# Performance work log

Measured on AMD Instinct MI355X. Metric: run time of the kernel, lower is better.

Reference implementation:

```python
import jax, jax.numpy as jnp
import numpy as np

DENSITY = 0.1  # fraction of nonzero weights kept by the mask


def setup_inputs() -> dict:
    key = jax.random.key(0)
    k_data, k_w, k_m, k_b = jax.random.split(key, 4)
    M, N, K = 8192, 4096, 4096  # tokens, out_features, in_features
    data = jax.random.normal(k_data, (M, K), dtype=jnp.float32)
    weight = jax.random.normal(k_w, (N, K), dtype=jnp.float32)
    mask = (jax.random.uniform(k_m, (N, K)) < DENSITY).astype(jnp.float32)
    bias = jax.random.normal(k_b, (N,), dtype=jnp.float32)
    return {"data": data, "weight": weight, "mask": mask, "bias": bias}


def reference(data, weight, mask, bias):
    # Equivalent to cuSPARSE CSR SpMM with W_sparse = mask * weight, plus bias:
    # out = data @ (mask * weight)^T + bias  (same math as ref_forward / F.linear)
    w = mask * weight  # [N, K]
    out = jnp.einsum('mk,nk->mn', data, w) + bias  # [M, N]
    return out
```

## Files before the change

### kernel.cpp

```cpp
#include <hip/hip_runtime.h>
#include <hip/hip_bf16.h>


#define Mdim 8192
#define Ndim 4096
#define Kdim 4096

typedef __bf16 bf16x8 __attribute__((ext_vector_type(8)));
typedef float f32x4 __attribute__((ext_vector_type(4)));

__device__ inline unsigned short f2bf(float f) {
    union { float f; unsigned u; } v;
    v.f = f;
    unsigned r = v.u + 0x7fffu + ((v.u >> 16) & 1u);
    return (unsigned short)(r >> 16);
}

__device__ inline unsigned pack2(float a, float b) {
    return (unsigned)f2bf(a) | ((unsigned)f2bf(b) << 16);
}

#define GLOAD_LDS16(gp, lp)                                                     \
    __builtin_amdgcn_global_load_lds((const __attribute__((address_space(1))) void*)(gp), \
                                     (__attribute__((address_space(3))) void*)(lp), 16, 0, 0)

__global__ __launch_bounds__(256) void k_cvt_all(const float4* __restrict__ data,
                                                 const float4* __restrict__ weight,
                                                 const float4* __restrict__ mask,
                                                 uint4* __restrict__ Abf,
                                                 uint4* __restrict__ Bbf) {
    const int NA = Mdim * (Kdim / 8);
    const int NB = Ndim * (Kdim / 8);
    const int stride = gridDim.x * blockDim.x;
    for (int i = blockIdx.x * blockDim.x + threadIdx.x; i < NA + NB; i += stride) {
        if (i < NA) {
            const size_t j2 = 2 * (size_t)i;
            float4 v0 = data[j2], v1 = data[j2 + 1];
            uint4 o;
            o.x = pack2(v0.x, v0.y); o.y = pack2(v0.z, v0.w);
            o.z = pack2(v1.x, v1.y); o.w = pack2(v1.z, v1.w);
            Abf[i] = o;
        } else {
            const size_t j = (size_t)(i - NA);
            const size_t j2 = 2 * j;
            float4 w0 = weight[j2], w1 = weight[j2 + 1];
            float4 m0 = mask[j2],   m1 = mask[j2 + 1];
            uint4 o;
            o.x = pack2(w0.x * m0.x, w0.y * m0.y);
            o.y = pack2(w0.z * m0.z, w0.w * m0.w);
            o.z = pack2(w1.x * m1.x, w1.y * m1.y);
            o.w = pack2(w1.z * m1.z, w1.w * m1.w);
            Bbf[j] = o;
        }
    }
}

__global__ __launch_bounds__(256) void k_gemm(const unsigned short* __restrict__ A,
                                              const unsigned short* __restrict__ B,
                                              const float* __restrict__ bias,
                                              float* __restrict__ out) {
    __shared__ unsigned short As[128 * 32];
    __shared__ unsigned short Bs[128 * 32];

    const int tid  = threadIdx.x;
    const int lane = tid & 63;
    const int wave = tid >> 6;
    const int wm   = (wave >> 1) * 64;
    const int wn   = (wave & 1) * 64;
    const int bm   = blockIdx.y * 128;
    const int bn   = blockIdx.x * 128;

    const int ar = lane >> 2;
    const int ac = (lane & 3) * 8;
    const unsigned short* Ag0 = A + (size_t)(bm + wave * 32 + ar) * Kdim + ac;
    const unsigned short* Ag1 = Ag0 + (size_t)16 * Kdim;
    const unsigned short* Bg0 = B + (size_t)(bn + wave * 32 + ar) * Kdim + ac;
    const unsigned short* Bg1 = Bg0 + (size_t)16 * Kdim;
    unsigned short* Al0 = As + wave * 1024 + lane * 8;
    unsigned short* Al1 = Al0 + 512;
    unsigned short* Bl0 = Bs + wave * 1024 + lane * 8;
    unsigned short* Bl1 = Bl0 + 512;

    f32x4 zero = {0.f, 0.f, 0.f, 0.f};
    f32x4 acc[4][4];
#pragma unroll
    for (int i = 0; i < 4; ++i)
#pragma unroll
        for (int j = 0; j < 4; ++j) acc[i][j] = zero;

    const int fr = lane & 15;
    const int fk = (lane >> 4) * 8;

    for (int k0 = 0; k0 < Kdim; k0 += 32) {
        GLOAD_LDS16(Ag0 + k0, Al0);
        GLOAD_LDS16(Ag1 + k0, Al1);
        GLOAD_LDS16(Bg0 + k0, Bl0);
        GLOAD_LDS16(Bg1 + k0, Bl1);
        __syncthreads();

        bf16x8 af[4], bfr[4];
#pragma unroll
        for (int i = 0; i < 4; ++i)
            af[i] = *(const bf16x8*)&As[(wm + i * 16 + fr) * 32 + fk];
#pragma unroll
        for (int j = 0; j < 4; ++j)
            bfr[j] = *(const bf16x8*)&Bs[(wn + j * 16 + fr) * 32 + fk];

#pragma unroll
        for (int i = 0; i < 4; ++i)
#pragma unroll
            for (int j = 0; j < 4; ++j)
                acc[i][j] = __builtin_amdgcn_mfma_f32_16x16x32_bf16(af[i], bfr[j], acc[i][j], 0, 0, 0);

        __syncthreads();
    }

    const int col_base = bn + wn + (lane & 15);
    const int row_base = bm + wm + (lane >> 4) * 4;
#pragma unroll
    for (int j = 0; j < 4; ++j) {
        const int col = col_base + j * 16;
        const float bv = bias[col];
#pragma unroll
        for (int i = 0; i < 4; ++i) {
            const int row = row_base + i * 16;
            float* op = out + (size_t)row * Ndim + col;
#pragma unroll
            for (int r = 0; r < 4; ++r) op[(size_t)r * Ndim] = acc[i][j][r] + bv;
        }
    }
}

__global__ void k_naive(const float* __restrict__ A, const float* __restrict__ W,
                        const float* __restrict__ Msk, const float* __restrict__ bias,
                        float* __restrict__ out) {
    int n = blockIdx.x * blockDim.x + threadIdx.x;
    int m = blockIdx.y;
    if (n >= Ndim) return;
    const float* a = A + (size_t)m * Kdim;
    const float* w = W + (size_t)n * Kdim;
    const float* mk = Msk + (size_t)n * Kdim;
    float s = 0.f;
    for (int k = 0; k < Kdim; ++k) s += a[k] * w[k] * mk[k];
    out[(size_t)m * Ndim + n] = s + bias[n];
}

extern "C" void kernel_launch(void* const* d_in, const int* in_sizes, int n_in,
                              void* d_out, int out_size, void* d_ws, size_t ws_size,
                              hipStream_t stream) {
    const float* data   = (const float*)d_in[0];
    const float* weight = (const float*)d_in[1];
    const float* mask   = (const float*)d_in[2];
    const float* bias   = (const float*)d_in[3];
    float* out = (float*)d_out;

    const size_t needA = (size_t)Mdim * Kdim * 2;
    const size_t needB = (size_t)Ndim * Kdim * 2;
    if (ws_size < needA + needB) {
        dim3 g((Ndim + 255) / 256, Mdim);
        k_naive<<<g, 256, 0, stream>>>(data, weight, mask, bias, out);
        return;
    }

    unsigned short* Abf = (unsigned short*)d_ws;
    unsigned short* Bbf = Abf + (size_t)Mdim * Kdim;

    k_cvt_all<<<4096, 256, 0, stream>>>((const float4*)data, (const float4*)weight,
                                        (const float4*)mask, (uint4*)Abf, (uint4*)Bbf);

    dim3 grid(Ndim / 128, Mdim / 128);
    k_gemm<<<grid, 256, 0, stream>>>(Abf, Bbf, bias, out);
}
```

Before: 621.3 us.

## Replace bf16 GEMM with 256x256 double-buffered, swizzled, pipelined MFMA kernel

The 128x128 single-buffered GEMM with BK=32 is replaced by a 512-thread kernel that computes a 256x256 tile with BK=64 and double-buffers its LDS. Global-to-LDS loads for the next K step are split into quarters and interleaved with MFMA phases, using explicit vmcnt waits, raw barriers and setprio. The LDS layout is XOR-swizzled to avoid bank conflicts, and the block index is remapped so neighbouring blocks share L2 tiles. The larger tile raises data reuse and arithmetic intensity, at the cost of 128 KB of LDS and high register pressure per block, and it relies on hand-counted vmcnt values being correct.

```diff
diff --git a/kernel.cpp b/kernel.cpp
--- a/kernel.cpp
+++ b/kernel.cpp
@@ -23,6 +23,10 @@
 #define GLOAD_LDS16(gp, lp)                                                     \
     __builtin_amdgcn_global_load_lds((const __attribute__((address_space(1))) void*)(gp), \
                                      (__attribute__((address_space(3))) void*)(lp), 16, 0, 0)
+
+#define VMCNT(n)  asm volatile("s_waitcnt vmcnt(" #n ")" ::: "memory")
+#define FENCE()   asm volatile("" ::: "memory")
+#define BARRIER() do { FENCE(); __builtin_amdgcn_s_barrier(); FENCE(); } while (0)
 
 __global__ __launch_bounds__(256) void k_cvt_all(const float4* __restrict__ data,
                                                  const float4* __restrict__ weight,
@@ -55,80 +59,174 @@
     }
 }
 
-__global__ __launch_bounds__(256) void k_gemm(const unsigned short* __restrict__ A,
-                                              const unsigned short* __restrict__ B,
-                                              const float* __restrict__ bias,
-                                              float* __restrict__ out) {
-    __shared__ unsigned short As[128 * 32];
-    __shared__ unsigned short Bs[128 * 32];
+__global__ __launch_bounds__(512, 2) void k_gemm256(const unsigned short* __restrict__ A,
+                                                    const unsigned short* __restrict__ B,
+                                                    const float* __restrict__ bias,
+                                                    float* __restrict__ out) {
+    __shared__ __align__(16) unsigned short sh[2 * 2 * 256 * 64];
 
     const int tid  = threadIdx.x;
     const int lane = tid & 63;
     const int wave = tid >> 6;
-    const int wm   = (wave >> 1) * 64;
-    const int wn   = (wave & 1) * 64;
-    const int bm   = blockIdx.y * 128;
-    const int bn   = blockIdx.x * 128;
-
-    const int ar = lane >> 2;
-    const int ac = (lane & 3) * 8;
-    const unsigned short* Ag0 = A + (size_t)(bm + wave * 32 + ar) * Kdim + ac;
-    const unsigned short* Ag1 = Ag0 + (size_t)16 * Kdim;
-    const unsigned short* Bg0 = B + (size_t)(bn + wave * 32 + ar) * Kdim + ac;
-    const unsigned short* Bg1 = Bg0 + (size_t)16 * Kdim;
-    unsigned short* Al0 = As + wave * 1024 + lane * 8;
-    unsigned short* Al1 = Al0 + 512;
-    unsigned short* Bl0 = Bs + wave * 1024 + lane * 8;
-    unsigned short* Bl1 = Bl0 + 512;
-
-    f32x4 zero = {0.f, 0.f, 0.f, 0.f};
-    f32x4 acc[4][4];
-#pragma unroll
-    for (int i = 0; i < 4; ++i)
-#pragma unroll
-        for (int j = 0; j < 4; ++j) acc[i][j] = zero;
+
+    const int bid = blockIdx.x;
+    const int swz = (bid & 7) * 64 + (bid >> 3);
+    const int bm  = (swz & 31) * 256;
+    const int bn  = (swz >> 5) * 256;
+
+    const int wm = (wave >> 2) * 128;
+    const int wn = (wave & 3) * 64;
+
+    const int rrow = lane >> 3;
+    const int scol = ((lane & 7) ^ rrow) * 8;
+    const int ldsl = lane * 8;
+    const int w8   = wave * 8;
+    const int rbB  = (wave >> 2) * 64 + (wave & 3) * 8;
 
     const int fr = lane & 15;
-    const int fk = (lane >> 4) * 8;
-
-    for (int k0 = 0; k0 < Kdim; k0 += 32) {
-        GLOAD_LDS16(Ag0 + k0, Al0);
-        GLOAD_LDS16(Ag1 + k0, Al1);
-        GLOAD_LDS16(Bg0 + k0, Bl0);
-        GLOAD_LDS16(Bg1 + k0, Bl1);
-        __syncthreads();
-
-        bf16x8 af[4], bfr[4];
-#pragma unroll
-        for (int i = 0; i < 4; ++i)
-            af[i] = *(const bf16x8*)&As[(wm + i * 16 + fr) * 32 + fk];
-#pragma unroll
-        for (int j = 0; j < 4; ++j)
-            bfr[j] = *(const bf16x8*)&Bs[(wn + j * 16 + fr) * 32 + fk];
-
-#pragma unroll
-        for (int i = 0; i < 4; ++i)
-#pragma unroll
-            for (int j = 0; j < 4; ++j)
-                acc[i][j] = __builtin_amdgcn_mfma_f32_16x16x32_bf16(af[i], bfr[j], acc[i][j], 0, 0, 0);
-
-        __syncthreads();
-    }
-
-    const int col_base = bn + wn + (lane & 15);
-    const int row_base = bm + wm + (lane >> 4) * 4;
-#pragma unroll
-    for (int j = 0; j < 4; ++j) {
-        const int col = col_base + j * 16;
+    const int kc = lane >> 4;
+    const int po = (kc ^ (fr & 7)) * 8;
+
+#define STAGE_A(buf, k0, Rb) GLOAD_LDS16(                                        \
+        A + (size_t)(bm + (Rb) + rrow) * Kdim + (k0) + scol,                     \
+        sh + (buf) * 32768 + (Rb) * 64 + ldsl)
+#define STAGE_B(buf, k0, Rb) GLOAD_LDS16(                                        \
+        B + (size_t)(bn + (Rb) + rrow) * Kdim + (k0) + scol,                     \
+        sh + (buf) * 32768 + 16384 + (Rb) * 64 + ldsl)
+
+    f32x4 acc[8][4];
+#pragma unroll
+    for (int i = 0; i < 8; ++i)
+#pragma unroll
+        for (int j = 0; j < 4; ++j) acc[i][j] = (f32x4){0.f, 0.f, 0.f, 0.f};
+
+    STAGE_A(0, 0, 0 + w8);   STAGE_A(0, 0, 128 + w8);
+    STAGE_B(0, 0, rbB);      STAGE_B(0, 0, rbB + 128);
+    STAGE_A(0, 0, 64 + w8);  STAGE_A(0, 0, 192 + w8);
+    STAGE_B(0, 0, rbB + 32); STAGE_B(0, 0, rbB + 160);
+    VMCNT(4);
+    BARRIER();
+
+#define MM(ci, cj, av, bv) \
+    acc[ci][cj] = __builtin_amdgcn_mfma_f32_16x16x32_bf16(av, bv, acc[ci][cj], 0, 0, 0)
+
+    const int NT = Kdim / 64;
+    for (int t = 0; t < NT - 1; ++t) {
+        const int cur  = t & 1;
+        const int nxtb = cur ^ 1;
+        const int k0n  = (t + 1) * 64;
+        const unsigned short* pA = sh + cur * 32768 + (wm + fr) * 64;
+        const unsigned short* pB = sh + cur * 32768 + 16384 + (wn + fr) * 64;
+
+        bf16x8 a0[4][2], a1[4][2], b0[2][2], b1[2][2];
+
+#pragma unroll
+        for (int i = 0; i < 4; ++i) {
+            a0[i][0] = *(const bf16x8*)(pA + i * 1024 + po);
+            a0[i][1] = *(const bf16x8*)(pA + i * 1024 + (po ^ 32));
+        }
+#pragma unroll
+        for (int j = 0; j < 2; ++j) {
+            b0[j][0] = *(const bf16x8*)(pB + j * 1024 + po);
+            b0[j][1] = *(const bf16x8*)(pB + j * 1024 + (po ^ 32));
+        }
+        STAGE_A(nxtb, k0n, 0 + w8); STAGE_A(nxtb, k0n, 128 + w8);
+        VMCNT(4);
+        BARRIER();
+        __builtin_amdgcn_s_setprio(1);
+#pragma unroll
+        for (int i = 0; i < 4; ++i)
+#pragma unroll
+            for (int j = 0; j < 2; ++j) { MM(i, j, a0[i][0], b0[j][0]); MM(i, j, a0[i][1], b0[j][1]); }
+        __builtin_amdgcn_s_setprio(0);
+
+#pragma unroll
+        for (int i = 0; i < 4; ++i) {
+            a1[i][0] = *(const bf16x8*)(pA + 4096 + i * 1024 + po);
+            a1[i][1] = *(const bf16x8*)(pA + 4096 + i * 1024 + (po ^ 32));
+        }
+        STAGE_B(nxtb, k0n, rbB); STAGE_B(nxtb, k0n, rbB + 128);
+        VMCNT(4);
+        BARRIER();
+        __builtin_amdgcn_s_setprio(1);
+#pragma unroll
+        for (int i = 0; i < 4; ++i)
+#pragma unroll
+            for (int j = 0; j < 2; ++j) { MM(4 + i, j, a1[i][0], b0[j][0]); MM(4 + i, j, a1[i][1], b0[j][1]); }
+        __builtin_amdgcn_s_setprio(0);
+
+#pragma unroll
+        for (int j = 0; j < 2; ++j) {
+            b1[j][0] = *(const bf16x8*)(pB + 2048 + j * 1024 + po);
+            b1[j][1] = *(const bf16x8*)(pB + 2048 + j * 1024 + (po ^ 32));
+        }
+        STAGE_A(nxtb, k0n, 64 + w8); STAGE_A(nxtb, k0n, 192 + w8);
+        __builtin_amdgcn_s_setprio(1);
+#pragma unroll
+        for (int i = 0; i < 4; ++i)
+#pragma unroll
+            for (int j = 0; j < 2; ++j) { MM(4 + i, 2 + j, a1[i][0], b1[j][0]); MM(4 + i, 2 + j, a1[i][1], b1[j][1]); }
+        __builtin_amdgcn_s_setprio(0);
+
+        STAGE_B(nxtb, k0n, rbB + 32); STAGE_B(nxtb, k0n, rbB + 160);
+        VMCNT(4);
+        BARRIER();
+        __builtin_amdgcn_s_setprio(1);
+#pragma unroll
+        for (int i = 0; i < 4; ++i)
+#pragma unroll
+            for (int j = 0; j < 2; ++j) { MM(i, 2 + j, a0[i][0], b1[j][0]); MM(i, 2 + j, a0[i][1], b1[j][1]); }
+        __builtin_amdgcn_s_setprio(0);
+    }
+
+    {
+        VMCNT(0);
+        BARRIER();
+        const unsigned short* pA = sh + 32768 + (wm + fr) * 64;
+        const unsigned short* pB = sh + 32768 + 16384 + (wn + fr) * 64;
+        bf16x8 a0[4][2], a1[4][2], b0[2][2], b1[2][2];
+#pragma unroll
+        for (int i = 0; i < 4; ++i) {
+            a0[i][0] = *(const bf16x8*)(pA + i * 1024 + po);
+            a0[i][1] = *(const bf16x8*)(pA + i * 1024 + (po ^ 32));
+            a1[i][0] = *(const bf16x8*)(pA + 4096 + i * 1024 + po);
+            a1[i][1] = *(const bf16x8*)(pA + 4096 + i * 1024 + (po ^ 32));
+        }
+#pragma unroll
+        for (int j = 0; j < 2; ++j) {
+            b0[j][0] = *(const bf16x8*)(pB + j * 1024 + po);
+            b0[j][1] = *(const bf16x8*)(pB + j * 1024 + (po ^ 32));
+            b1[j][0] = *(const bf16x8*)(pB + 2048 + j * 1024 + po);
+            b1[j][1] = *(const bf16x8*)(pB + 2048 + j * 1024 + (po ^ 32));
+        }
+#pragma unroll
+        for (int i = 0; i < 4; ++i)
+#pragma unroll
+            for (int j = 0; j < 2; ++j) {
+                MM(i, j, a0[i][0], b0[j][0]);         MM(i, j, a0[i][1], b0[j][1]);
+                MM(4 + i, j, a1[i][0], b0[j][0]);     MM(4 + i, j, a1[i][1], b0[j][1]);
+                MM(4 + i, 2 + j, a1[i][0], b1[j][0]); MM(4 + i, 2 + j, a1[i][1], b1[j][1]);
+                MM(i, 2 + j, a0[i][0], b1[j][0]);     MM(i, 2 + j, a0[i][1], b1[j][1]);
+            }
+    }
+
+    const int colb = bn + wn + fr;
+    const int rowb = bm + wm + (lane >> 4) * 4;
+#pragma unroll
+    for (int jg = 0; jg < 4; ++jg) {
+        const int col = colb + jg * 16;
         const float bv = bias[col];
 #pragma unroll
-        for (int i = 0; i < 4; ++i) {
-            const int row = row_base + i * 16;
+        for (int ig = 0; ig < 8; ++ig) {
+            const int row = rowb + ig * 16;
             float* op = out + (size_t)row * Ndim + col;
 #pragma unroll
-            for (int r = 0; r < 4; ++r) op[(size_t)r * Ndim] = acc[i][j][r] + bv;
-        }
-    }
+            for (int r = 0; r < 4; ++r) op[(size_t)r * Ndim] = acc[ig][jg][r] + bv;
+        }
+    }
+#undef MM
+#undef STAGE_A
+#undef STAGE_B
 }
 
 __global__ void k_naive(const float* __restrict__ A, const float* __restrict__ W,
@@ -168,6 +266,5 @@
     k_cvt_all<<<4096, 256, 0, stream>>>((const float4*)data, (const float4*)weight,
                                         (const float4*)mask, (uint4*)Abf, (uint4*)Bbf);
 
-    dim3 grid(Ndim / 128, Mdim / 128);
-    k_gemm<<<grid, 256, 0, stream>>>(Abf, Bbf, bias, out);
-}
+    k_gemm256<<<dim3(512), dim3(512), 0, stream>>>(Abf, Bbf, bias, out);
+}
```

Measured after the change: 557.5 us. 1.11x faster.
